# Kernel tuning notes

Measured on AMD Instinct MI355X. Metric: run time of the kernel, lower is better.

The kernel has to match this reference:

```python
import jax, jax.numpy as jnp
import numpy as np

ALPHA = 0.1  # CELU alpha used by ANI networks


def setup_inputs() -> dict:
    key = jax.random.key(0)
    ks = jax.random.split(key, 10)
    B, A, S = 1024, 256, 4            # molecules, atoms, species
    sizes = [384, 256, 192, 160, 1]   # aev_size followed by MLP layer sizes
    inp = {
        "fullaev": jax.random.normal(ks[0], (B, A, sizes[0]), dtype=jnp.float32),
        "species": jax.random.randint(ks[1], (A,), 0, S, dtype=jnp.int32),
    }
    for j in range(4):
        fan_in = sizes[j]
        scale = 1.0 / np.sqrt(fan_in).astype(np.float32)
        inp[f"W{j}"] = jax.random.normal(ks[2 + 2 * j], (S, sizes[j], sizes[j + 1]), dtype=jnp.float32) * scale
        inp[f"b{j}"] = jax.random.uniform(ks[3 + 2 * j], (S, sizes[j + 1]), dtype=jnp.float32, minval=-scale, maxval=scale)
    return inp


def reference(fullaev, species, W0, b0, W1, b1, W2, b2, W3, b3):
    # Per-atom species-routed MLP: atom i uses weights of expert species[i].
    # Gathered-weight einsum == grouped GEMM over atoms (MoE-style dispatch).
    def layer(y, W, b):
        Wa = W[species]          # [A, in, out] per-atom expert weights
        ba = b[species]          # [A, out]
        y = jnp.einsum('bai,aio->bao', y, Wa) + ba[None, :, :]
        return jax.nn.celu(y, alpha=ALPHA)

    y = fullaev                  # [B, A, aev]
    for W, b in ((W0, b0), (W1, b1), (W2, b2), (W3, b3)):
        y = layer(y, W, b)       # activation after every layer, incl. last (as in source)
    mol = jnp.sum(y, axis=1)     # sum-pool over atoms -> [B, 1]
    return jnp.squeeze(mol)      # -> [B]
```

## Files before the change

### kernel.cpp

```cpp
#include <hip/hip_runtime.h>
#include <stdint.h>


typedef _Float16 f16;
typedef _Float16 f16x8 __attribute__((ext_vector_type(8)));
typedef _Float16 f16x4 __attribute__((ext_vector_type(4)));
typedef float f32x16 __attribute__((ext_vector_type(16)));

static constexpr int BMOL = 1024;
static constexpr int NATOM = 256;
static constexpr int TB = 64;

static constexpr size_t PK0 = 0;
static constexpr size_t PK1 = PK0 + 4 * (size_t)98304;
static constexpr size_t PK2 = PK1 + 4 * (size_t)49152;
static constexpr size_t PK3 = PK2 + 4 * (size_t)36864;

static constexpr int OFF_ACT0 = 0;
static constexpr int OFF_ACT1 = 33792;
static constexpr int OFF_XBUF = 33792;
static constexpr int OFF_WBUF = 59392;
static constexpr int OFF_BIAS = 75776;
static constexpr int OFF_W3   = 76800;
static constexpr int SMEM_BYTES = 77184;

__device__ __forceinline__ float celu_f(float x) {
    float e = __expf(x * 10.0f);
    return fmaxf(x, 0.0f) + fminf(0.0f, 0.1f * (e - 1.0f));
}

__global__ void pack_weights(const float* __restrict__ W0, const float* __restrict__ W1,
                             const float* __restrict__ W2, const float* __restrict__ W3,
                             f16* __restrict__ wp)
{
    const int layer = blockIdx.y;
    int K, Nreal, NT, E; const float* W; size_t base;
    if (layer == 0)      { K = 384; Nreal = 256; NT = 8; E = 98304; W = W0; base = PK0; }
    else if (layer == 1) { K = 256; Nreal = 192; NT = 6; E = 49152; W = W1; base = PK1; }
    else if (layer == 2) { K = 192; Nreal = 160; NT = 6; E = 36864; W = W2; base = PK2; }
    else                 { K = 160; Nreal = 1;   NT = 1; E = 160;   W = W3; base = PK3; }
    const int total = 4 * E;
    for (int p = blockIdx.x * blockDim.x + threadIdx.x; p < total; p += gridDim.x * blockDim.x) {
        const int s = p / E, q = p - s * E;
        if (layer == 3) { wp[base + p] = (f16)W[s * 160 + q]; continue; }
        const int j = q & 7, l = (q >> 3) & 63, r = q >> 9;
        const int nt = r % NT, ks = r / NT;
        const int k = ks * 16 + ((l >> 5) << 3) + j;
        const int o = nt * 32 + (l & 31);
        const float v = (o < Nreal) ? W[(s * K + k) * Nreal + o] : 0.0f;
        wp[base + p] = (f16)v;
    }
}

__device__ __forceinline__ void loadx8(float* d, const float* p) {
    float4 u = *(const float4*)p;
    float4 v = *(const float4*)(p + 4);
    d[0]=u.x; d[1]=u.y; d[2]=u.z; d[3]=u.w; d[4]=v.x; d[5]=v.y; d[6]=v.z; d[7]=v.w;
}
__device__ __forceinline__ void writex8(char* xb, int row, int kq, const float* v) {
    f16x8 h;
#pragma unroll
    for (int i = 0; i < 8; i++) h[i] = (f16)v[i];
    *(f16x8*)(xb + row * 80 + kq * 2) = h;
}

template<int NT>
__device__ __forceinline__ void wload(uint2* wr, const f16* wsrc, int ks, int t) {
    const uint2* p = (const uint2*)wsrc + (size_t)ks * NT * 128 + t;
#pragma unroll
    for (int i = 0; i < NT / 2; i++) wr[i] = p[i * 256];
}
template<int NT>
__device__ __forceinline__ void wwrite(const uint2* wr, char* dst, int t) {
    uint2* p = (uint2*)dst + t;
#pragma unroll
    for (int i = 0; i < NT / 2; i++) p[i * 256] = wr[i];
}

template<int NT>
__device__ __forceinline__ void mfma_step(const char* actbase, int strideB, int kByteOff,
                                          const char* wslab, int l, int w, f32x16 acc[2][2]) {
    const int lo = l & 31, hi = l >> 5;
    f16x8 af0 = *(const f16x8*)(actbase + lo * strideB + kByteOff + hi * 16);
    f16x8 af1 = *(const f16x8*)(actbase + (32 + lo) * strideB + kByteOff + hi * 16);
#pragma unroll
    for (int ni = 0; ni < 2; ni++) {
        const int nt = w + ni * 4;
        if (nt < NT) {
            f16x8 wf = *(const f16x8*)(wslab + (nt * 64 + l) * 16);
            acc[ni][0] = __builtin_amdgcn_mfma_f32_32x32x16_f16(wf, af0, acc[ni][0], 0, 0, 0);
            acc[ni][1] = __builtin_amdgcn_mfma_f32_32x32x16_f16(wf, af1, acc[ni][1], 0, 0, 0);
        }
    }
}

template<int NT>
__device__ __forceinline__ void epilogue(f32x16 acc[2][2], char* actout, int strideB,
                                         const float* biasL, int l, int w) {
    const int lo = l & 31, hi = l >> 5;
#pragma unroll
    for (int ni = 0; ni < 2; ni++) {
        const int nt = w + ni * 4;
        if (nt >= NT) continue;
#pragma unroll
        for (int mi = 0; mi < 2; mi++) {
            const int row = mi * 32 + lo;
#pragma unroll
            for (int q = 0; q < 4; q++) {
                const int o = nt * 32 + q * 8 + hi * 4;
                float4 bv = *(const float4*)(biasL + o);
                const float* bp = (const float*)&bv;
                f16x4 hv;
#pragma unroll
                for (int d = 0; d < 4; d++) {
                    float v = acc[ni][mi][q * 4 + d] + bp[d];
                    hv[d] = (f16)celu_f(v);
                }
                *(f16x4*)(actout + row * strideB + o * 2) = hv;
            }
        }
    }
}

template<int KS, int NT>
__device__ __forceinline__ void gemm_lds(const char* actin, int sin, char* actout, int sout,
                                         const f16* wsrc, const float* bsrc, int Nreal, int sp,
                                         char* wbuf, float* biasL, int t, int l, int w,
                                         f32x16 acc[2][2]) {
    for (int o = t; o < NT * 32; o += 256) biasL[o] = (o < Nreal) ? bsrc[sp * Nreal + o] : 0.0f;
#pragma unroll
    for (int ni = 0; ni < 2; ni++)
#pragma unroll
        for (int mi = 0; mi < 2; mi++)
#pragma unroll
            for (int e = 0; e < 16; e++) acc[ni][mi][e] = 0.0f;

    uint2 wreg[4];
    wload<NT>(wreg, wsrc, 0, t);
    wwrite<NT>(wreg, wbuf, t);
    __syncthreads();
    for (int ks = 0; ks < KS; ks++) {
        if (ks + 1 < KS) wload<NT>(wreg, wsrc, ks + 1, t);
        mfma_step<NT>(actin, sin, ks * 32, wbuf + (ks & 1) * (NT * 1024), l, w, acc);
        if (ks + 1 < KS) wwrite<NT>(wreg, wbuf + ((ks + 1) & 1) * (NT * 1024), t);
        __syncthreads();
    }
    epilogue<NT>(acc, actout, sout, biasL, l, w);
    __syncthreads();
}

__global__ void __launch_bounds__(256, 2)
ani_kernel(const float* __restrict__ X, const int* __restrict__ species,
           const float* __restrict__ B0, const float* __restrict__ B1,
           const float* __restrict__ B2, const float* __restrict__ B3,
           const f16* __restrict__ wp, float* __restrict__ out)
{
    __shared__ __align__(16) char smem[SMEM_BYTES];
    char* act0 = smem + OFF_ACT0;
    char* act1 = smem + OFF_ACT1;
    char* act2 = smem + OFF_ACT0;
    char* xbuf = smem + OFF_XBUF;
    char* wbuf = smem + OFF_WBUF;
    float* biasL = (float*)(smem + OFF_BIAS);
    f16* w3l = (f16*)(smem + OFF_W3);

    const int t = threadIdx.x, l = t & 63, w = t >> 6;
    const int atom = blockIdx.y;
    const long brow0 = (long)blockIdx.x * TB;
    const int sp = species[atom];

    if (t < 160) w3l[t] = wp[PK3 + sp * 160 + t];

    f32x16 acc[2][2];

    {
        constexpr int NT = 8, KS = 24, NC = 12;
        const f16* wsrc = wp + PK0 + (size_t)sp * 98304;
        if (t < 256) biasL[t] = B0[sp * 256 + t];

        const int xrow_i = t >> 2, kq = (t & 3) * 8;
        const float* xrow = X + ((brow0 + xrow_i) * (long)NATOM + atom) * 384 + kq;

        float xr[2][8];
        uint2 wreg[4];
#pragma unroll
        for (int ni = 0; ni < 2; ni++)
#pragma unroll
            for (int mi = 0; mi < 2; mi++)
#pragma unroll
                for (int e = 0; e < 16; e++) acc[ni][mi][e] = 0.0f;

        loadx8(xr[0], xrow);
        loadx8(xr[1], xrow + 32);
        wload<NT>(wreg, wsrc, 0, t);
        writex8(xbuf, xrow_i, kq, xr[0]);
        wwrite<NT>(wreg, wbuf, t);
        __syncthreads();

        for (int ks = 0; ks < KS; ks++) {
            const int c = ks >> 1, h = ks & 1;
            if (ks + 1 < KS) wload<NT>(wreg, wsrc, ks + 1, t);
            mfma_step<NT>(xbuf + (c & 1) * 5120, 80, h * 32, wbuf + (ks & 1) * 8192, l, w, acc);
            if (ks + 1 < KS) wwrite<NT>(wreg, wbuf + ((ks + 1) & 1) * 8192, t);
            if (h == 1) {
                if (c + 1 < NC) writex8(xbuf + ((c + 1) & 1) * 5120, xrow_i, kq, xr[(c + 1) & 1]);
                if (c + 2 < NC) loadx8(xr[c & 1], xrow + (c + 2) * 32);
            }
            __syncthreads();
        }
        epilogue<NT>(acc, act0, 528, biasL, l, w);
        __syncthreads();
    }

    gemm_lds<16, 6>(act0, 528, act1, 400, wp + PK1 + (size_t)sp * 49152, B1, 192, sp,
                    wbuf, biasL, t, l, w, acc);

    gemm_lds<12, 6>(act1, 400, act2, 400, wp + PK2 + (size_t)sp * 36864, B2, 160, sp,
                    wbuf, biasL, t, l, w, acc);

    {
        const int row = t >> 2, part = t & 3;
        const char* arow = act2 + row * 400 + part * 80;
        const f16* wrow = w3l + part * 40;
        float sum = 0.0f;
#pragma unroll
        for (int g = 0; g < 5; g++) {
            f16x8 a = *(const f16x8*)(arow + g * 16);
            f16x8 wv = *(const f16x8*)(wrow + g * 8);
#pragma unroll
            for (int e = 0; e < 8; e++) sum += (float)a[e] * (float)wv[e];
        }
        sum += __shfl_xor(sum, 1, 64);
        sum += __shfl_xor(sum, 2, 64);
        if (part == 0) {
            float y = celu_f(sum + B3[sp]);
            atomicAdd(out + brow0 + row, y);
        }
    }
}

extern "C" void kernel_launch(void* const* d_in, const int* in_sizes, int n_in,
                              void* d_out, int out_size, void* d_ws, size_t ws_size,
                              hipStream_t stream)
{
    const float* X  = (const float*)d_in[0];
    const int* spc  = (const int*)d_in[1];
    const float* W0 = (const float*)d_in[2];
    const float* b0 = (const float*)d_in[3];
    const float* W1 = (const float*)d_in[4];
    const float* b1 = (const float*)d_in[5];
    const float* W2 = (const float*)d_in[6];
    const float* b2 = (const float*)d_in[7];
    const float* W3 = (const float*)d_in[8];
    const float* b3 = (const float*)d_in[9];
    f16* wp = (f16*)d_ws;
    float* out = (float*)d_out;

    hipMemsetAsync(d_out, 0, (size_t)out_size * sizeof(float), stream);
    pack_weights<<<dim3(512, 4), 256, 0, stream>>>(W0, W1, W2, W3, wp);
    ani_kernel<<<dim3(BMOL / TB, NATOM), 256, 0, stream>>>(X, spc, b0, b1, b2, b3, wp, out);
}
```

Measured before the change: 713.1 us.

## Stream weight fragments directly from global into registers, dropping LDS weight staging

Weight fragments are now loaded per wave straight from global/L2 into registers with one-step register prefetch, instead of being staged through a double-buffered LDS slab with a barrier every k-step. The layer-0 X staging moves to a triple buffer so only one barrier per 32-wide chunk is needed, and the wave-to-tile mapping is reassigned (each wave owns two N-tiles in layer 0, and one M-half with three N-tiles in later layers). Bias and last-layer weights are read from global rather than LDS, which shrinks shared memory and may allow more occupancy. In exchange, every wave re-reads weight fragments from cache, raising L2 traffic, and register pressure grows.

Result: faster. 681.6 us (-4.4%).

```diff
diff --git a/kernel.cpp b/kernel.cpp
--- a/kernel.cpp
+++ b/kernel.cpp
@@ -7,49 +7,49 @@
 typedef _Float16 f16x4 __attribute__((ext_vector_type(4)));
 typedef float f32x16 __attribute__((ext_vector_type(16)));
 
-static constexpr int BMOL = 1024;
 static constexpr int NATOM = 256;
-static constexpr int TB = 64;
+static constexpr int BMOL  = 1024;
+static constexpr int TB    = 64;
 
 static constexpr size_t PK0 = 0;
 static constexpr size_t PK1 = PK0 + 4 * (size_t)98304;
 static constexpr size_t PK2 = PK1 + 4 * (size_t)49152;
 static constexpr size_t PK3 = PK2 + 4 * (size_t)36864;
 
+static constexpr int S_ACT0   = 528;
+static constexpr int S_ACT1   = 400;
 static constexpr int OFF_ACT0 = 0;
-static constexpr int OFF_ACT1 = 33792;
-static constexpr int OFF_XBUF = 33792;
-static constexpr int OFF_WBUF = 59392;
-static constexpr int OFF_BIAS = 75776;
-static constexpr int OFF_W3   = 76800;
-static constexpr int SMEM_BYTES = 77184;
+static constexpr int OFF_ACT1 = 64 * S_ACT0;
+static constexpr int OFF_XBUF = OFF_ACT1;
+static constexpr int SMEM_BYTES = OFF_ACT1 + 64 * S_ACT1;
 
 __device__ __forceinline__ float celu_f(float x) {
     float e = __expf(x * 10.0f);
     return fmaxf(x, 0.0f) + fminf(0.0f, 0.1f * (e - 1.0f));
 }
 
+template<int K, int Nreal, int NT, int E>
+__device__ __forceinline__ void pack_one(const float* __restrict__ W, f16* __restrict__ dst,
+                                         int tid, int nth) {
+    for (int p = tid; p < 4 * E; p += nth) {
+        const int s = p / E, q = p - s * E;
+        const int j = q & 7, ll = (q >> 3) & 63, r = q >> 9;
+        const int nt = r % NT, ks = r / NT;
+        const int k = ks * 16 + ((ll >> 5) << 3) + j;
+        const int o = nt * 32 + (ll & 31);
+        const float v = (o < Nreal) ? W[((size_t)s * K + k) * Nreal + o] : 0.0f;
+        dst[p] = (f16)v;
+    }
+}
+
 __global__ void pack_weights(const float* __restrict__ W0, const float* __restrict__ W1,
                              const float* __restrict__ W2, const float* __restrict__ W3,
-                             f16* __restrict__ wp)
-{
-    const int layer = blockIdx.y;
-    int K, Nreal, NT, E; const float* W; size_t base;
-    if (layer == 0)      { K = 384; Nreal = 256; NT = 8; E = 98304; W = W0; base = PK0; }
-    else if (layer == 1) { K = 256; Nreal = 192; NT = 6; E = 49152; W = W1; base = PK1; }
-    else if (layer == 2) { K = 192; Nreal = 160; NT = 6; E = 36864; W = W2; base = PK2; }
-    else                 { K = 160; Nreal = 1;   NT = 1; E = 160;   W = W3; base = PK3; }
-    const int total = 4 * E;
-    for (int p = blockIdx.x * blockDim.x + threadIdx.x; p < total; p += gridDim.x * blockDim.x) {
-        const int s = p / E, q = p - s * E;
-        if (layer == 3) { wp[base + p] = (f16)W[s * 160 + q]; continue; }
-        const int j = q & 7, l = (q >> 3) & 63, r = q >> 9;
-        const int nt = r % NT, ks = r / NT;
-        const int k = ks * 16 + ((l >> 5) << 3) + j;
-        const int o = nt * 32 + (l & 31);
-        const float v = (o < Nreal) ? W[(s * K + k) * Nreal + o] : 0.0f;
-        wp[base + p] = (f16)v;
-    }
+                             f16* __restrict__ wp) {
+    const int tid = blockIdx.x * 256 + threadIdx.x, nth = gridDim.x * 256;
+    if      (blockIdx.y == 0) pack_one<384, 256, 8, 98304>(W0, wp + PK0, tid, nth);
+    else if (blockIdx.y == 1) pack_one<256, 192, 6, 49152>(W1, wp + PK1, tid, nth);
+    else if (blockIdx.y == 2) pack_one<192, 160, 6, 36864>(W2, wp + PK2, tid, nth);
+    else { for (int p = tid; p < 640; p += nth) wp[PK3 + p] = (f16)W3[p]; }
 }
 
 __device__ __forceinline__ void loadx8(float* d, const float* p) {
@@ -64,89 +64,49 @@
     *(f16x8*)(xb + row * 80 + kq * 2) = h;
 }
 
-template<int NT>
-__device__ __forceinline__ void wload(uint2* wr, const f16* wsrc, int ks, int t) {
-    const uint2* p = (const uint2*)wsrc + (size_t)ks * NT * 128 + t;
-#pragma unroll
-    for (int i = 0; i < NT / 2; i++) wr[i] = p[i * 256];
-}
-template<int NT>
-__device__ __forceinline__ void wwrite(const uint2* wr, char* dst, int t) {
-    uint2* p = (uint2*)dst + t;
-#pragma unroll
-    for (int i = 0; i < NT / 2; i++) p[i * 256] = wr[i];
-}
-
-template<int NT>
-__device__ __forceinline__ void mfma_step(const char* actbase, int strideB, int kByteOff,
-                                          const char* wslab, int l, int w, f32x16 acc[2][2]) {
-    const int lo = l & 31, hi = l >> 5;
-    f16x8 af0 = *(const f16x8*)(actbase + lo * strideB + kByteOff + hi * 16);
-    f16x8 af1 = *(const f16x8*)(actbase + (32 + lo) * strideB + kByteOff + hi * 16);
-#pragma unroll
-    for (int ni = 0; ni < 2; ni++) {
-        const int nt = w + ni * 4;
-        if (nt < NT) {
-            f16x8 wf = *(const f16x8*)(wslab + (nt * 64 + l) * 16);
-            acc[ni][0] = __builtin_amdgcn_mfma_f32_32x32x16_f16(wf, af0, acc[ni][0], 0, 0, 0);
-            acc[ni][1] = __builtin_amdgcn_mfma_f32_32x32x16_f16(wf, af1, acc[ni][1], 0, 0, 0);
-        }
-    }
-}
-
-template<int NT>
-__device__ __forceinline__ void epilogue(f32x16 acc[2][2], char* actout, int strideB,
-                                         const float* biasL, int l, int w) {
-    const int lo = l & 31, hi = l >> 5;
-#pragma unroll
-    for (int ni = 0; ni < 2; ni++) {
-        const int nt = w + ni * 4;
-        if (nt >= NT) continue;
-#pragma unroll
-        for (int mi = 0; mi < 2; mi++) {
-            const int row = mi * 32 + lo;
-#pragma unroll
-            for (int q = 0; q < 4; q++) {
-                const int o = nt * 32 + q * 8 + hi * 4;
-                float4 bv = *(const float4*)(biasL + o);
-                const float* bp = (const float*)&bv;
-                f16x4 hv;
-#pragma unroll
-                for (int d = 0; d < 4; d++) {
-                    float v = acc[ni][mi][q * 4 + d] + bp[d];
-                    hv[d] = (f16)celu_f(v);
-                }
-                *(f16x4*)(actout + row * strideB + o * 2) = hv;
-            }
-        }
+__device__ __forceinline__ f16x8 wfrag(const f16* __restrict__ w, int ks, int NT, int nt, int l) {
+    return *(const f16x8*)(w + (((size_t)ks * NT + nt) * 64 + l) * 8);
+}
+
+__device__ __forceinline__ void epi_store(const f32x16& a, int nt, int mi, char* actout,
+                                          int strideB, const float* __restrict__ bias_sp,
+                                          int Nreal, int lo, int hi) {
+    if (nt * 32 >= Nreal) return;
+    const int row = mi * 32 + lo;
+#pragma unroll
+    for (int q = 0; q < 4; q++) {
+        const int o = nt * 32 + q * 8 + hi * 4;
+        float4 bv = *(const float4*)(bias_sp + o);
+        const float* bp = (const float*)&bv;
+        f16x4 hv;
+#pragma unroll
+        for (int d = 0; d < 4; d++) hv[d] = (f16)celu_f(a[q * 4 + d] + bp[d]);
+        *(f16x4*)(actout + row * strideB + o * 2) = hv;
     }
 }
 
 template<int KS, int NT>
-__device__ __forceinline__ void gemm_lds(const char* actin, int sin, char* actout, int sout,
-                                         const f16* wsrc, const float* bsrc, int Nreal, int sp,
-                                         char* wbuf, float* biasL, int t, int l, int w,
-                                         f32x16 acc[2][2]) {
-    for (int o = t; o < NT * 32; o += 256) biasL[o] = (o < Nreal) ? bsrc[sp * Nreal + o] : 0.0f;
-#pragma unroll
-    for (int ni = 0; ni < 2; ni++)
-#pragma unroll
-        for (int mi = 0; mi < 2; mi++)
-#pragma unroll
-            for (int e = 0; e < 16; e++) acc[ni][mi][e] = 0.0f;
-
-    uint2 wreg[4];
-    wload<NT>(wreg, wsrc, 0, t);
-    wwrite<NT>(wreg, wbuf, t);
-    __syncthreads();
+__device__ __forceinline__ void gemm_str(const char* actin, int sin, const f16* __restrict__ wsrc,
+                                         int l, int lo, int hi, int w, f32x16* acc) {
+    const int mi = w & 1, nt0 = w >> 1;
+    const char* arow = actin + (mi * 32 + lo) * sin + hi * 16;
+    f16x8 wf0 = wfrag(wsrc, 0, NT, nt0,     l);
+    f16x8 wf1 = wfrag(wsrc, 0, NT, nt0 + 2, l);
+    f16x8 wf2 = wfrag(wsrc, 0, NT, nt0 + 4, l);
+#pragma unroll
     for (int ks = 0; ks < KS; ks++) {
-        if (ks + 1 < KS) wload<NT>(wreg, wsrc, ks + 1, t);
-        mfma_step<NT>(actin, sin, ks * 32, wbuf + (ks & 1) * (NT * 1024), l, w, acc);
-        if (ks + 1 < KS) wwrite<NT>(wreg, wbuf + ((ks + 1) & 1) * (NT * 1024), t);
-        __syncthreads();
-    }
-    epilogue<NT>(acc, actout, sout, biasL, l, w);
-    __syncthreads();
+        f16x8 n0, n1, n2;
+        if (ks + 1 < KS) {
+            n0 = wfrag(wsrc, ks + 1, NT, nt0,     l);
+            n1 = wfrag(wsrc, ks + 1, NT, nt0 + 2, l);
+            n2 = wfrag(wsrc, ks + 1, NT, nt0 + 4, l);
+        }
+        f16x8 af = *(const f16x8*)(arow + ks * 32);
+        acc[0] = __builtin_amdgcn_mfma_f32_32x32x16_f16(wf0, af, acc[0], 0, 0, 0);
+        acc[1] = __builtin_amdgcn_mfma_f32_32x32x16_f16(wf1, af, acc[1], 0, 0, 0);
+        acc[2] = __builtin_amdgcn_mfma_f32_32x32x16_f16(wf2, af, acc[2], 0, 0, 0);
+        wf0 = n0; wf1 = n1; wf2 = n2;
+    }
 }
 
 __global__ void __launch_bounds__(256, 2)
@@ -160,72 +120,103 @@
     char* act1 = smem + OFF_ACT1;
     char* act2 = smem + OFF_ACT0;
     char* xbuf = smem + OFF_XBUF;
-    char* wbuf = smem + OFF_WBUF;
-    float* biasL = (float*)(smem + OFF_BIAS);
-    f16* w3l = (f16*)(smem + OFF_W3);
-
-    const int t = threadIdx.x, l = t & 63, w = t >> 6;
+
+    const int t = threadIdx.x, l = t & 63, w = t >> 6, lo = l & 31, hi = l >> 5;
     const int atom = blockIdx.y;
     const long brow0 = (long)blockIdx.x * TB;
     const int sp = species[atom];
 
-    if (t < 160) w3l[t] = wp[PK3 + sp * 160 + t];
-
-    f32x16 acc[2][2];
-
-    {
-        constexpr int NT = 8, KS = 24, NC = 12;
+    f32x16 acc[4];
+
+    {
         const f16* wsrc = wp + PK0 + (size_t)sp * 98304;
-        if (t < 256) biasL[t] = B0[sp * 256 + t];
-
-        const int xrow_i = t >> 2, kq = (t & 3) * 8;
-        const float* xrow = X + ((brow0 + xrow_i) * (long)NATOM + atom) * 384 + kq;
+        const int xri = t >> 2, kq = (t & 3) * 8;
+        const float* xrow = X + ((brow0 + xri) * (long)NATOM + atom) * 384 + kq;
 
         float xr[2][8];
-        uint2 wreg[4];
-#pragma unroll
-        for (int ni = 0; ni < 2; ni++)
-#pragma unroll
-            for (int mi = 0; mi < 2; mi++)
-#pragma unroll
-                for (int e = 0; e < 16; e++) acc[ni][mi][e] = 0.0f;
-
         loadx8(xr[0], xrow);
         loadx8(xr[1], xrow + 32);
-        wload<NT>(wreg, wsrc, 0, t);
-        writex8(xbuf, xrow_i, kq, xr[0]);
-        wwrite<NT>(wreg, wbuf, t);
+        writex8(xbuf, xri, kq, xr[0]);
+        f16x8 wc0 = wfrag(wsrc, 0, 8, 2 * w,     l);
+        f16x8 wc1 = wfrag(wsrc, 0, 8, 2 * w + 1, l);
+        f16x8 wc2 = wfrag(wsrc, 1, 8, 2 * w,     l);
+        f16x8 wc3 = wfrag(wsrc, 1, 8, 2 * w + 1, l);
+#pragma unroll
+        for (int i = 0; i < 4; i++)
+#pragma unroll
+            for (int e = 0; e < 16; e++) acc[i][e] = 0.0f;
+
+#pragma unroll
+        for (int c = 0; c < 12; c++) {
+            if (c + 1 < 12) writex8(xbuf + ((c + 1) % 3) * 5120, xri, kq, xr[(c + 1) & 1]);
+            __syncthreads();
+            if (c + 2 < 12) loadx8(xr[c & 1], xrow + (c + 2) * 32);
+            f16x8 wn0, wn1, wn2, wn3;
+            if (c + 1 < 12) {
+                wn0 = wfrag(wsrc, 2 * c + 2, 8, 2 * w,     l);
+                wn1 = wfrag(wsrc, 2 * c + 2, 8, 2 * w + 1, l);
+                wn2 = wfrag(wsrc, 2 * c + 3, 8, 2 * w,     l);
+                wn3 = wfrag(wsrc, 2 * c + 3, 8, 2 * w + 1, l);
+            }
+            const char* xb = xbuf + (c % 3) * 5120;
+            f16x8 a00 = *(const f16x8*)(xb + lo * 80 + hi * 16);
+            f16x8 a01 = *(const f16x8*)(xb + (32 + lo) * 80 + hi * 16);
+            acc[0] = __builtin_amdgcn_mfma_f32_32x32x16_f16(wc0, a00, acc[0], 0, 0, 0);
+            acc[1] = __builtin_amdgcn_mfma_f32_32x32x16_f16(wc0, a01, acc[1], 0, 0, 0);
+            acc[2] = __builtin_amdgcn_mfma_f32_32x32x16_f16(wc1, a00, acc[2], 0, 0, 0);
+            acc[3] = __builtin_amdgcn_mfma_f32_32x32x16_f16(wc1, a01, acc[3], 0, 0, 0);
+            f16x8 a10 = *(const f16x8*)(xb + lo * 80 + 32 + hi * 16);
+            f16x8 a11 = *(const f16x8*)(xb + (32 + lo) * 80 + 32 + hi * 16);
+            acc[0] = __builtin_amdgcn_mfma_f32_32x32x16_f16(wc2, a10, acc[0], 0, 0, 0);
+            acc[1] = __builtin_amdgcn_mfma_f32_32x32x16_f16(wc2, a11, acc[1], 0, 0, 0);
+            acc[2] = __builtin_amdgcn_mfma_f32_32x32x16_f16(wc3, a10, acc[2], 0, 0, 0);
+            acc[3] = __builtin_amdgcn_mfma_f32_32x32x16_f16(wc3, a11, acc[3], 0, 0, 0);
+            wc0 = wn0; wc1 = wn1; wc2 = wn2; wc3 = wn3;
+        }
+        const float* bias0 = B0 + sp * 256;
+        epi_store(acc[0], 2 * w,     0, act0, S_ACT0, bias0, 256, lo, hi);
+        epi_store(acc[1], 2 * w,     1, act0, S_ACT0, bias0, 256, lo, hi);
+        epi_store(acc[2], 2 * w + 1, 0, act0, S_ACT0, bias0, 256, lo, hi);
+        epi_store(acc[3], 2 * w + 1, 1, act0, S_ACT0, bias0, 256, lo, hi);
         __syncthreads();
-
-        for (int ks = 0; ks < KS; ks++) {
-            const int c = ks >> 1, h = ks & 1;
-            if (ks + 1 < KS) wload<NT>(wreg, wsrc, ks + 1, t);
-            mfma_step<NT>(xbuf + (c & 1) * 5120, 80, h * 32, wbuf + (ks & 1) * 8192, l, w, acc);
-            if (ks + 1 < KS) wwrite<NT>(wreg, wbuf + ((ks + 1) & 1) * 8192, t);
-            if (h == 1) {
-                if (c + 1 < NC) writex8(xbuf + ((c + 1) & 1) * 5120, xrow_i, kq, xr[(c + 1) & 1]);
-                if (c + 2 < NC) loadx8(xr[c & 1], xrow + (c + 2) * 32);
-            }
-            __syncthreads();
-        }
-        epilogue<NT>(acc, act0, 528, biasL, l, w);
+    }
+
+    {
+#pragma unroll
+        for (int i = 0; i < 3; i++)
+#pragma unroll
+            for (int e = 0; e < 16; e++) acc[i][e] = 0.0f;
+        gemm_str<16, 6>(act0, S_ACT0, wp + PK1 + (size_t)sp * 49152, l, lo, hi, w, acc);
+        const float* bias1 = B1 + sp * 192;
+        const int nt0 = w >> 1, mi = w & 1;
+        epi_store(acc[0], nt0,     mi, act1, S_ACT1, bias1, 192, lo, hi);
+        epi_store(acc[1], nt0 + 2, mi, act1, S_ACT1, bias1, 192, lo, hi);
+        epi_store(acc[2], nt0 + 4, mi, act1, S_ACT1, bias1, 192, lo, hi);
         __syncthreads();
     }
 
-    gemm_lds<16, 6>(act0, 528, act1, 400, wp + PK1 + (size_t)sp * 49152, B1, 192, sp,
-                    wbuf, biasL, t, l, w, acc);
-
-    gemm_lds<12, 6>(act1, 400, act2, 400, wp + PK2 + (size_t)sp * 36864, B2, 160, sp,
-                    wbuf, biasL, t, l, w, acc);
+    {
+#pragma unroll
+        for (int i = 0; i < 3; i++)
+#pragma unroll
+            for (int e = 0; e < 16; e++) acc[i][e] = 0.0f;
+        gemm_str<12, 6>(act1, S_ACT1, wp + PK2 + (size_t)sp * 36864, l, lo, hi, w, acc);
+        const float* bias2 = B2 + sp * 160;
+        const int nt0 = w >> 1, mi = w & 1;
+        epi_store(acc[0], nt0,     mi, act2, S_ACT1, bias2, 160, lo, hi);
+        epi_store(acc[1], nt0 + 2, mi, act2, S_ACT1, bias2, 160, lo, hi);
+        epi_store(acc[2], nt0 + 4, mi, act2, S_ACT1, bias2, 160, lo, hi);
+        __syncthreads();
+    }
 
     {
         const int row = t >> 2, part = t & 3;
-        const char* arow = act2 + row * 400 + part * 80;
-        const f16* wrow = w3l + part * 40;
+        const char* arow = act2 + row * S_ACT1 + part * 80;
+        const f16* wrow = wp + PK3 + sp * 160 + part * 40;
         float sum = 0.0f;
 #pragma unroll
         for (int g = 0; g < 5; g++) {
-            f16x8 a = *(const f16x8*)(arow + g * 16);
+            f16x8 a  = *(const f16x8*)(arow + g * 16);
             f16x8 wv = *(const f16x8*)(wrow + g * 8);
 #pragma unroll
             for (int e = 0; e < 8; e++) sum += (float)a[e] * (float)wv[e];
@@ -233,8 +224,7 @@
         sum += __shfl_xor(sum, 1, 64);
         sum += __shfl_xor(sum, 2, 64);
         if (part == 0) {
-            float y = celu_f(sum + B3[sp]);
-            atomicAdd(out + brow0 + row, y);
+            atomicAdd(out + brow0 + row, celu_f(sum + B3[sp]));
         }
     }
 }
@@ -257,6 +247,6 @@
     float* out = (float*)d_out;
 
     hipMemsetAsync(d_out, 0, (size_t)out_size * sizeof(float), stream);
-    pack_weights<<<dim3(512, 4), 256, 0, stream>>>(W0, W1, W2, W3, wp);
+    pack_weights<<<dim3(256, 4), 256, 0, stream>>>(W0, W1, W2, W3, wp);
     ani_kernel<<<dim3(BMOL / TB, NATOM), 256, 0, stream>>>(X, spc, b0, b1, b2, b3, wp, out);
 }
```
